# Performance work log

Hardware: AMD Instinct MI355X
Metric: run time of the kernel (lower is better)

## Reference

```python
import jax, jax.numpy as jnp
import numpy as np

D_MODEL = 1024
N_HEADS = 16
HEAD_DIM = D_MODEL // N_HEADS


def setup_inputs() -> dict:
    key = jax.random.key(0)
    ks = jax.random.split(key, 5)
    T, B = 2048, 2
    x = jax.random.normal(ks[0], (T, B, D_MODEL), dtype=jnp.float32)
    s = 1.0 / np.sqrt(D_MODEL)
    Wq = jax.random.normal(ks[1], (D_MODEL, D_MODEL), dtype=jnp.float32) * s
    Wk = jax.random.normal(ks[2], (D_MODEL, D_MODEL), dtype=jnp.float32) * s
    Wv = jax.random.normal(ks[3], (D_MODEL, D_MODEL), dtype=jnp.float32) * s
    Wo = jax.random.normal(ks[4], (D_MODEL, D_MODEL), dtype=jnp.float32) * s
    return {"x": x, "Wq": Wq, "Wk": Wk, "Wv": Wv, "Wo": Wo}


def reference(x, Wq, Wk, Wv, Wo):
    T, B, C = x.shape
    H, D = N_HEADS, HEAD_DIM

    def split_heads(t):
        # (T,B,C) -> (B,H,T,D), matching view+permute(1,2,0,3)
        return t.reshape(T, B, H, D).transpose(1, 2, 0, 3)

    q = split_heads(x @ Wq.T)
    k = split_heads(x @ Wk.T)
    v = split_heads(x @ Wv.T)

    scale = 1.0 / jnp.sqrt(jnp.asarray(D, dtype=x.dtype))
    scores = jnp.einsum('bhqd,bhkd->bhqk', q, k) * scale  # (B,H,T,T)
    causal = jnp.tril(jnp.ones((T, T), dtype=bool))
    scores = jnp.where(causal, scores, jnp.asarray(-jnp.inf, dtype=scores.dtype))
    probs = jax.nn.softmax(scores, axis=-1)
    ctx = jnp.einsum('bhqk,bhkd->bhqd', probs, v)  # (B,H,T,D)
    ctx = ctx.transpose(2, 0, 1, 3).reshape(T, B, C)
    return ctx @ Wo.T
```

## Files before the change

### kernel.cpp

```cpp
#include <hip/hip_runtime.h>
#include <hip/hip_bf16.h>

#define TT 2048
#define BB 2
#define CC 1024
#define HH 16
#define DD 64
#define MM (TT * BB)

typedef short bf16x8 __attribute__((ext_vector_type(8)));
typedef float f32x4  __attribute__((ext_vector_type(4)));

__device__ inline ushort f2b(float f) {
    union { float f; unsigned u; } v; v.f = f;
    unsigned r = v.u + 0x7FFFu + ((v.u >> 16) & 1u);
    return (ushort)(r >> 16);
}

__device__ inline unsigned pack_bf16(float a, float b) {
    __hip_bfloat162 h = __float22bfloat162_rn(make_float2(a, b));
    union { __hip_bfloat162 h; unsigned u; } c; c.h = h;
    return c.u;
}

__device__ inline void gload_lds16(const ushort* g, ushort* l) {
    __builtin_amdgcn_global_load_lds(
        (const __attribute__((address_space(1))) void*)g,
        (__attribute__((address_space(3))) void*)l, 16, 0, 0);
}

#define XQUADS (MM * CC / 4)
#define WQUADS (CC * CC / 4)
__global__ __launch_bounds__(256) void conv_all(const float* __restrict__ x,
                                                const float* __restrict__ Wq,
                                                const float* __restrict__ Wk,
                                                const float* __restrict__ Wv,
                                                const float* __restrict__ Wo,
                                                ushort* __restrict__ dst) {
    int idx = blockIdx.x * 256 + threadIdx.x;
    const float* src;
    int off;
    if (idx < XQUADS) {
        src = x; off = idx;
    } else {
        int wi = (idx - XQUADS) >> 18;
        off = (idx - XQUADS) & (WQUADS - 1);
        src = (wi == 0) ? Wq : (wi == 1) ? Wk : (wi == 2) ? Wv : Wo;
    }
    float4 v = ((const float4*)src)[off];
    ushort4 o = {f2b(v.x), f2b(v.y), f2b(v.z), f2b(v.w)};
    ((ushort4*)dst)[idx] = o;
}

__global__ __launch_bounds__(256) void gemm_qkv(const ushort* __restrict__ A,
                                                const ushort* __restrict__ B0,
                                                const ushort* __restrict__ B1,
                                                const ushort* __restrict__ B2,
                                                ushort* __restrict__ Oq,
                                                ushort* __restrict__ Ok,
                                                ushort* __restrict__ Ov) {
    __shared__ __align__(16) ushort As[128 * 32];
    __shared__ __align__(16) ushort Bs[128 * 32];

    const int tid = threadIdx.x;
    const int wave = tid >> 6, lane = tid & 63;
    const int quad = lane >> 4, l16 = lane & 15;
    const int wm = wave >> 1, wn = wave & 1;

    const int bm = blockIdx.x * 128;
    const int by = blockIdx.y;
    const int wsel = by >> 3;
    const ushort* Bp = (wsel == 0) ? B0 : (wsel == 1) ? B1 : B2;
    const int bn = (by & 7) * 128;

    const int srow = lane >> 2;
    const int scol = (lane & 3) * 8;

    f32x4 acc[4][4];
#pragma unroll
    for (int i = 0; i < 4; i++)
#pragma unroll
        for (int j = 0; j < 4; j++) acc[i][j] = (f32x4){0.f, 0.f, 0.f, 0.f};

    for (int k0 = 0; k0 < CC; k0 += 32) {
#pragma unroll
        for (int i = 0; i < 2; i++) {
            const int rbase = wave * 32 + i * 16;
            gload_lds16(A + (size_t)(bm + rbase + srow) * CC + k0 + scol,
                        As + rbase * 32);
            gload_lds16(Bp + (size_t)(bn + rbase + srow) * CC + k0 + scol,
                        Bs + rbase * 32);
        }
        __syncthreads();

        bf16x8 af[4], bf[4];
#pragma unroll
        for (int mi = 0; mi < 4; mi++)
            af[mi] = *(const bf16x8*)(As + (wm * 64 + mi * 16 + l16) * 32 + quad * 8);
#pragma unroll
        for (int ni = 0; ni < 4; ni++)
            bf[ni] = *(const bf16x8*)(Bs + (wn * 64 + ni * 16 + l16) * 32 + quad * 8);
#pragma unroll
        for (int mi = 0; mi < 4; mi++)
#pragma unroll
            for (int ni = 0; ni < 4; ni++)
                acc[mi][ni] = __builtin_amdgcn_mfma_f32_16x16x32_bf16(
                    af[mi], bf[ni], acc[mi][ni], 0, 0, 0);
        __syncthreads();
    }

#pragma unroll
    for (int mi = 0; mi < 4; mi++) {
#pragma unroll
        for (int r = 0; r < 4; r++) {
            const int m = bm + wm * 64 + mi * 16 + quad * 4 + r;
#pragma unroll
            for (int ni = 0; ni < 4; ni++) {
                const int colg = bn + wn * 64 + ni * 16 + l16;
                float v = acc[mi][ni][r];
                if (wsel == 0) v *= 0.18033688f;
                const int t = m >> 1, b = m & 1;
                const int h = colg >> 6, d = colg & 63;
                ushort* dst = (wsel == 0) ? Oq : (wsel == 1) ? Ok : Ov;
                dst[(((size_t)(b * HH + h)) * TT + t) * DD + d] = f2b(v);
            }
        }
    }
}

__global__ __launch_bounds__(256) void gemm_out(const ushort* __restrict__ A,
                                                const ushort* __restrict__ Bm,
                                                float* __restrict__ Of) {
    __shared__ __align__(16) ushort As[128 * 32];
    __shared__ __align__(16) ushort Bs[64 * 32];

    const int tid = threadIdx.x;
    const int wave = tid >> 6, lane = tid & 63;
    const int quad = lane >> 4, l16 = lane & 15;

    const int bm = blockIdx.x * 128;
    const int bn = blockIdx.y * 64;

    const int srow = lane >> 2;
    const int scol = (lane & 3) * 8;

    f32x4 acc[2][4];
#pragma unroll
    for (int i = 0; i < 2; i++)
#pragma unroll
        for (int j = 0; j < 4; j++) acc[i][j] = (f32x4){0.f, 0.f, 0.f, 0.f};

    for (int k0 = 0; k0 < CC; k0 += 32) {
#pragma unroll
        for (int i = 0; i < 2; i++) {
            const int rbase = wave * 32 + i * 16;
            gload_lds16(A + (size_t)(bm + rbase + srow) * CC + k0 + scol,
                        As + rbase * 32);
        }
        gload_lds16(Bm + (size_t)(bn + wave * 16 + srow) * CC + k0 + scol,
                    Bs + wave * 16 * 32);
        __syncthreads();

        bf16x8 af[2], bf[4];
#pragma unroll
        for (int mi = 0; mi < 2; mi++)
            af[mi] = *(const bf16x8*)(As + (wave * 32 + mi * 16 + l16) * 32 + quad * 8);
#pragma unroll
        for (int ni = 0; ni < 4; ni++)
            bf[ni] = *(const bf16x8*)(Bs + (ni * 16 + l16) * 32 + quad * 8);
#pragma unroll
        for (int mi = 0; mi < 2; mi++)
#pragma unroll
            for (int ni = 0; ni < 4; ni++)
                acc[mi][ni] = __builtin_amdgcn_mfma_f32_16x16x32_bf16(
                    af[mi], bf[ni], acc[mi][ni], 0, 0, 0);
        __syncthreads();
    }

#pragma unroll
    for (int mi = 0; mi < 2; mi++)
#pragma unroll
        for (int r = 0; r < 4; r++) {
            const int m = bm + wave * 32 + mi * 16 + quad * 4 + r;
#pragma unroll
            for (int ni = 0; ni < 4; ni++)
                Of[(size_t)m * CC + bn + ni * 16 + l16] = acc[mi][ni][r];
        }
}

__global__ __launch_bounds__(256) void prep_kv(const ushort* __restrict__ Kb,
                                               const ushort* __restrict__ Vb,
                                               ushort* __restrict__ Kf,
                                               ushort* __restrict__ Vf) {
    __shared__ __align__(16) ushort Ls[64 * 72];
    const int tile = blockIdx.x;
    const int bh   = blockIdx.y;
    const int t    = threadIdx.x;
    const size_t src = (size_t)bh * TT * DD + (size_t)tile * 64 * DD;
    const size_t dst = (size_t)bh * TT * DD + (size_t)tile * 4096;

#pragma unroll
    for (int i = 0; i < 2; i++) {
        int e = t + i * 256;
        int r = e >> 3, kc = (e & 7) * 8;
        *(uint4*)(Ls + r * 72 + kc) = *(const uint4*)(Kb + src + r * 64 + kc);
    }
    __syncthreads();
#pragma unroll
    for (int i = 0; i < 2; i++) {
        int o = t + i * 256;
        int c = o >> 8, nb = (o >> 6) & 3, lane = o & 63;
        int quad = lane >> 4, l16 = lane & 15;
        int j = nb * 16 + l16, k0 = c * 32 + quad * 8;
        *(uint4*)(Kf + dst + (size_t)o * 8) = *(const uint4*)(Ls + j * 72 + k0);
    }
    __syncthreads();

#pragma unroll
    for (int i = 0; i < 2; i++) {
        int e = t + i * 256;
        int r = e >> 3, kc = (e & 7) * 8;
        *(uint4*)(Ls + r * 72 + kc) = *(const uint4*)(Vb + src + r * 64 + kc);
    }
    __syncthreads();
#pragma unroll
    for (int i = 0; i < 2; i++) {
        int o = t + i * 256;
        int c = o >> 8, db = (o >> 6) & 3, lane = o & 63;
        int quad = lane >> 4, l16 = lane & 15;
        int d = db * 16 + l16;
        ushort tmp[8];
#pragma unroll
        for (int u = 0; u < 8; u++) {
            int jp = c * 32 + quad * 8 + u;
            int j = (jp & 3) * 16 + (jp >> 2);
            tmp[u] = Ls[j * 72 + d];
        }
        *(uint4*)(Vf + dst + (size_t)o * 8) = *(uint4*)tmp;
    }
}

template <bool DIAG>
__device__ __forceinline__ void attn_step(const bf16x8* qa, f32x4* O, float* l,
                                          const bf16x8* kf, const bf16x8* vf,
                                          ushort* P, int j0, int qbase,
                                          int quad, int l16) {
    f32x4 S[4];
#pragma unroll
    for (int nb = 0; nb < 4; nb++) S[nb] = (f32x4){0.f, 0.f, 0.f, 0.f};
#pragma unroll
    for (int c = 0; c < 2; c++)
#pragma unroll
        for (int nb = 0; nb < 4; nb++)
            S[nb] = __builtin_amdgcn_mfma_f32_16x16x32_bf16(qa[c], kf[c * 4 + nb],
                                                            S[nb], 0, 0, 0);

#pragma unroll
    for (int r = 0; r < 4; r++) {
        const int qg = qbase + quad * 4 + r;
        float p[4];
#pragma unroll
        for (int nb = 0; nb < 4; nb++) {
            float s = S[nb][r];
            if (DIAG) { if (j0 + nb * 16 + l16 > qg) s = -1e30f; }
            p[nb] = __builtin_amdgcn_exp2f(s);
        }
        l[r] += (p[0] + p[1]) + (p[2] + p[3]);
        uint2 w; w.x = pack_bf16(p[0], p[1]); w.y = pack_bf16(p[2], p[3]);
        *(uint2*)(P + (quad * 4 + r) * 72 + l16 * 4) = w;
    }

#pragma unroll
    for (int c = 0; c < 2; c++) {
        bf16x8 pa = *(const bf16x8*)(P + l16 * 72 + c * 32 + quad * 8);
#pragma unroll
        for (int db = 0; db < 4; db++)
            O[db] = __builtin_amdgcn_mfma_f32_16x16x32_bf16(pa, vf[c * 4 + db],
                                                            O[db], 0, 0, 0);
    }
}

__global__ __launch_bounds__(256, 2) void attn_mfma(const ushort* __restrict__ Qb,
                                                    const ushort* __restrict__ Kf,
                                                    const ushort* __restrict__ Vf,
                                                    ushort* __restrict__ ctx) {
    __shared__ __align__(16) ushort PsA[4 * 16 * 72];
    __shared__ __align__(16) ushort PsB[4 * 16 * 72];

    const int tid  = threadIdx.x;
    const int wave = tid >> 6;
    const int lane = tid & 63;
    const int quad = lane >> 4;
    const int l16  = lane & 15;

    const int p  = blockIdx.x;
    const int bh = blockIdx.y;
    const int qtA = p, qtB = (TT / 64 - 1) - p;
    const int q0A = qtA * 64 + wave * 16;
    const int q0B = qtB * 64 + wave * 16;

    const size_t baseQK = (size_t)bh * TT * DD;

    bf16x8 qaA[2], qaB[2];
    {
        const ushort* qp = Qb + baseQK + (size_t)(q0A + l16) * DD + quad * 8;
        qaA[0] = *(const bf16x8*)(qp);
        qaA[1] = *(const bf16x8*)(qp + 32);
        const ushort* qp2 = Qb + baseQK + (size_t)(q0B + l16) * DD + quad * 8;
        qaB[0] = *(const bf16x8*)(qp2);
        qaB[1] = *(const bf16x8*)(qp2 + 32);
    }

    f32x4 OA[4], OB[4];
#pragma unroll
    for (int i = 0; i < 4; i++) {
        OA[i] = (f32x4){0.f, 0.f, 0.f, 0.f};
        OB[i] = (f32x4){0.f, 0.f, 0.f, 0.f};
    }
    float lA[4] = {0.f, 0.f, 0.f, 0.f};
    float lB[4] = {0.f, 0.f, 0.f, 0.f};

    ushort* PA = PsA + wave * 16 * 72;
    ushort* PB = PsB + wave * 16 * 72;

    const ushort* Kfp = Kf + baseQK;
    const ushort* Vfp = Vf + baseQK;

    for (int kt = 0; kt <= qtB; kt++) {
        const int j0 = kt * 64;

        bf16x8 kf[8], vf[8];
#pragma unroll
        for (int i = 0; i < 8; i++) {
            kf[i] = *(const bf16x8*)(Kfp + (i << 9) + lane * 8);
            vf[i] = *(const bf16x8*)(Vfp + (i << 9) + lane * 8);
        }

        if (kt == qtB)
            attn_step<true >(qaB, OB, lB, kf, vf, PB, j0, q0B, quad, l16);
        else
            attn_step<false>(qaB, OB, lB, kf, vf, PB, j0, q0B, quad, l16);

        if (kt < qtA)
            attn_step<false>(qaA, OA, lA, kf, vf, PA, j0, q0A, quad, l16);
        else if (kt == qtA)
            attn_step<true >(qaA, OA, lA, kf, vf, PA, j0, q0A, quad, l16);

        Kfp += 4096;
        Vfp += 4096;
    }

    const int b = bh >> 4, h = bh & 15;
#pragma unroll
    for (int r = 0; r < 4; r++) {
        float la = lA[r], lb = lB[r];
        la += __shfl_xor(la, 1); la += __shfl_xor(la, 2);
        la += __shfl_xor(la, 4); la += __shfl_xor(la, 8);
        lb += __shfl_xor(lb, 1); lb += __shfl_xor(lb, 2);
        lb += __shfl_xor(lb, 4); lb += __shfl_xor(lb, 8);
        const float invA = 1.f / la;
        const float invB = 1.f / lb;
        const int tA = q0A + quad * 4 + r;
        const int tB = q0B + quad * 4 + r;
#pragma unroll
        for (int db = 0; db < 4; db++) {
            ctx[((size_t)tA * BB + b) * CC + h * DD + db * 16 + l16] =
                f2b(OA[db][r] * invA);
            ctx[((size_t)tB * BB + b) * CC + h * DD + db * 16 + l16] =
                f2b(OB[db][r] * invB);
        }
    }
}

extern "C" void kernel_launch(void* const* d_in, const int* in_sizes, int n_in,
                              void* d_out, int out_size, void* d_ws, size_t ws_size,
                              hipStream_t stream) {
    const float* x  = (const float*)d_in[0];
    const float* Wq = (const float*)d_in[1];
    const float* Wk = (const float*)d_in[2];
    const float* Wv = (const float*)d_in[3];
    const float* Wo = (const float*)d_in[4];
    float* out = (float*)d_out;

    ushort* xb  = (ushort*)d_ws;
    ushort* Wb  = xb + (size_t)MM * CC;
    ushort* Wqb = Wb;
    ushort* Wkb = Wb + (size_t)CC * CC;
    ushort* Wvb = Wb + 2 * (size_t)CC * CC;
    ushort* Wob = Wb + 3 * (size_t)CC * CC;
    ushort* Qb  = Wb + 4 * (size_t)CC * CC;
    ushort* Kb  = Qb + (size_t)MM * CC;
    ushort* Vb  = Kb + (size_t)MM * CC;
    ushort* Kf  = Vb + (size_t)MM * CC;
    ushort* Vf  = Kf + (size_t)MM * CC;
    ushort* Ctxb = Vf + (size_t)MM * CC;

    conv_all<<<dim3((XQUADS + 4 * WQUADS) / 256), 256, 0, stream>>>(
        x, Wq, Wk, Wv, Wo, xb);

    gemm_qkv<<<dim3(MM / 128, 24), 256, 0, stream>>>(
        xb, Wqb, Wkb, Wvb, Qb, Kb, Vb);

    prep_kv<<<dim3(TT / 64, BB * HH), 256, 0, stream>>>(Kb, Vb, Kf, Vf);

    attn_mfma<<<dim3(TT / 128, BB * HH), 256, 0, stream>>>(Qb, Kf, Vf, Ctxb);

    gemm_out<<<dim3(MM / 128, CC / 64), 256, 0, stream>>>(Ctxb, Wob, out);
}
```

Before: 176.2 us.

## Write K in fragment layout from QKV GEMM and enlarge attention query tiles

The QKV GEMM epilogue now writes K directly in the MFMA fragment layout, so prep only rearranges V and the separate K transpose pass is dropped. The attention kernel now gives each wave 32 query rows per tile (128 per block tile), which halves the grid to 8x32 blocks and doubles reuse of each loaded K/V fragment. It also prefetches the next K tile into registers while the current one is used. The cost is more register pressure (launch bounds drop to 1 block per CU), fewer blocks to spread across the GPU, and scattered K stores in the GEMM epilogue.

New measurement: 185.3 us. +5.2%, slower.

```diff
diff --git a/kernel.cpp b/kernel.cpp
--- a/kernel.cpp
+++ b/kernel.cpp
@@ -118,11 +118,21 @@
             for (int ni = 0; ni < 4; ni++) {
                 const int colg = bn + wn * 64 + ni * 16 + l16;
                 float v = acc[mi][ni][r];
-                if (wsel == 0) v *= 0.18033688f;
                 const int t = m >> 1, b = m & 1;
                 const int h = colg >> 6, d = colg & 63;
-                ushort* dst = (wsel == 0) ? Oq : (wsel == 1) ? Ok : Ov;
-                dst[(((size_t)(b * HH + h)) * TT + t) * DD + d] = f2b(v);
+                if (wsel == 0) {
+                    v *= 0.18033688f;
+                    Oq[(((size_t)(b * HH + h)) * TT + t) * DD + d] = f2b(v);
+                } else if (wsel == 1) {
+                    const int jj = t & 63;
+                    size_t idx = ((size_t)(b * HH + h) * TT) * DD
+                               + (size_t)(t >> 6) * 4096
+                               + (d >> 5) * 2048 + (jj >> 4) * 512
+                               + (((d >> 3) & 3) * 16 + (jj & 15)) * 8 + (d & 7);
+                    Ok[idx] = f2b(v);
+                } else {
+                    Ov[(((size_t)(b * HH + h)) * TT + t) * DD + d] = f2b(v);
+                }
             }
         }
     }
@@ -188,10 +198,8 @@
         }
 }
 
-__global__ __launch_bounds__(256) void prep_kv(const ushort* __restrict__ Kb,
-                                               const ushort* __restrict__ Vb,
-                                               ushort* __restrict__ Kf,
-                                               ushort* __restrict__ Vf) {
+__global__ __launch_bounds__(256) void prep_v(const ushort* __restrict__ Vb,
+                                              ushort* __restrict__ Vf) {
     __shared__ __align__(16) ushort Ls[64 * 72];
     const int tile = blockIdx.x;
     const int bh   = blockIdx.y;
@@ -203,23 +211,6 @@
     for (int i = 0; i < 2; i++) {
         int e = t + i * 256;
         int r = e >> 3, kc = (e & 7) * 8;
-        *(uint4*)(Ls + r * 72 + kc) = *(const uint4*)(Kb + src + r * 64 + kc);
-    }
-    __syncthreads();
-#pragma unroll
-    for (int i = 0; i < 2; i++) {
-        int o = t + i * 256;
-        int c = o >> 8, nb = (o >> 6) & 3, lane = o & 63;
-        int quad = lane >> 4, l16 = lane & 15;
-        int j = nb * 16 + l16, k0 = c * 32 + quad * 8;
-        *(uint4*)(Kf + dst + (size_t)o * 8) = *(const uint4*)(Ls + j * 72 + k0);
-    }
-    __syncthreads();
-
-#pragma unroll
-    for (int i = 0; i < 2; i++) {
-        int e = t + i * 256;
-        int r = e >> 3, kc = (e & 7) * 8;
         *(uint4*)(Ls + r * 72 + kc) = *(const uint4*)(Vb + src + r * 64 + kc);
     }
     __syncthreads();
@@ -240,136 +231,186 @@
     }
 }
 
-template <bool DIAG>
-__device__ __forceinline__ void attn_step(const bf16x8* qa, f32x4* O, float* l,
-                                          const bf16x8* kf, const bf16x8* vf,
-                                          ushort* P, int j0, int qbase,
-                                          int quad, int l16) {
-    f32x4 S[4];
-#pragma unroll
-    for (int nb = 0; nb < 4; nb++) S[nb] = (f32x4){0.f, 0.f, 0.f, 0.f};
-#pragma unroll
-    for (int c = 0; c < 2; c++)
-#pragma unroll
-        for (int nb = 0; nb < 4; nb++)
-            S[nb] = __builtin_amdgcn_mfma_f32_16x16x32_bf16(qa[c], kf[c * 4 + nb],
-                                                            S[nb], 0, 0, 0);
-
-#pragma unroll
-    for (int r = 0; r < 4; r++) {
-        const int qg = qbase + quad * 4 + r;
-        float p[4];
-#pragma unroll
-        for (int nb = 0; nb < 4; nb++) {
-            float s = S[nb][r];
-            if (DIAG) { if (j0 + nb * 16 + l16 > qg) s = -1e30f; }
-            p[nb] = __builtin_amdgcn_exp2f(s);
-        }
-        l[r] += (p[0] + p[1]) + (p[2] + p[3]);
-        uint2 w; w.x = pack_bf16(p[0], p[1]); w.y = pack_bf16(p[2], p[3]);
-        *(uint2*)(P + (quad * 4 + r) * 72 + l16 * 4) = w;
-    }
-
-#pragma unroll
-    for (int c = 0; c < 2; c++) {
-        bf16x8 pa = *(const bf16x8*)(P + l16 * 72 + c * 32 + quad * 8);
-#pragma unroll
-        for (int db = 0; db < 4; db++)
-            O[db] = __builtin_amdgcn_mfma_f32_16x16x32_bf16(pa, vf[c * 4 + db],
-                                                            O[db], 0, 0, 0);
-    }
-}
-
-__global__ __launch_bounds__(256, 2) void attn_mfma(const ushort* __restrict__ Qb,
+__global__ __launch_bounds__(256, 1) void attn_mfma(const ushort* __restrict__ Qb,
                                                     const ushort* __restrict__ Kf,
                                                     const ushort* __restrict__ Vf,
                                                     ushort* __restrict__ ctx) {
-    __shared__ __align__(16) ushort PsA[4 * 16 * 72];
-    __shared__ __align__(16) ushort PsB[4 * 16 * 72];
+    __shared__ __align__(16) ushort PsA[4 * 32 * 72];
+    __shared__ __align__(16) ushort PsB[4 * 32 * 72];
 
     const int tid  = threadIdx.x;
-    const int wave = tid >> 6;
+    const int wave = __builtin_amdgcn_readfirstlane(tid >> 6);
     const int lane = tid & 63;
     const int quad = lane >> 4;
     const int l16  = lane & 15;
 
     const int p  = blockIdx.x;
     const int bh = blockIdx.y;
-    const int qtA = p, qtB = (TT / 64 - 1) - p;
-    const int q0A = qtA * 64 + wave * 16;
-    const int q0B = qtB * 64 + wave * 16;
+    const int qtA = p, qtB = 15 - p;
+    const int q0A = qtA * 128 + wave * 32;
+    const int q0B = qtB * 128 + wave * 32;
+    const int kdA = q0A >> 6;
+    const int kdB = q0B >> 6;
 
     const size_t baseQK = (size_t)bh * TT * DD;
 
-    bf16x8 qaA[2], qaB[2];
-    {
-        const ushort* qp = Qb + baseQK + (size_t)(q0A + l16) * DD + quad * 8;
-        qaA[0] = *(const bf16x8*)(qp);
-        qaA[1] = *(const bf16x8*)(qp + 32);
-        const ushort* qp2 = Qb + baseQK + (size_t)(q0B + l16) * DD + quad * 8;
-        qaB[0] = *(const bf16x8*)(qp2);
-        qaB[1] = *(const bf16x8*)(qp2 + 32);
-    }
-
-    f32x4 OA[4], OB[4];
-#pragma unroll
-    for (int i = 0; i < 4; i++) {
-        OA[i] = (f32x4){0.f, 0.f, 0.f, 0.f};
-        OB[i] = (f32x4){0.f, 0.f, 0.f, 0.f};
-    }
-    float lA[4] = {0.f, 0.f, 0.f, 0.f};
-    float lB[4] = {0.f, 0.f, 0.f, 0.f};
-
-    ushort* PA = PsA + wave * 16 * 72;
-    ushort* PB = PsB + wave * 16 * 72;
+    bf16x8 qaA[2][2], qaB[2][2];
+#pragma unroll
+    for (int ms = 0; ms < 2; ms++) {
+        const ushort* qp = Qb + baseQK + (size_t)(q0A + ms * 16 + l16) * DD + quad * 8;
+        qaA[ms][0] = *(const bf16x8*)(qp);
+        qaA[ms][1] = *(const bf16x8*)(qp + 32);
+        const ushort* qp2 = Qb + baseQK + (size_t)(q0B + ms * 16 + l16) * DD + quad * 8;
+        qaB[ms][0] = *(const bf16x8*)(qp2);
+        qaB[ms][1] = *(const bf16x8*)(qp2 + 32);
+    }
+
+    f32x4 OA[2][4], OB[2][4];
+#pragma unroll
+    for (int ms = 0; ms < 2; ms++)
+#pragma unroll
+        for (int db = 0; db < 4; db++) {
+            OA[ms][db] = (f32x4){0.f, 0.f, 0.f, 0.f};
+            OB[ms][db] = (f32x4){0.f, 0.f, 0.f, 0.f};
+        }
+    float lA[2][4] = {{0.f}}, lB[2][4] = {{0.f}};
+
+    ushort* PA = PsA + wave * 32 * 72;
+    ushort* PB = PsB + wave * 32 * 72;
 
     const ushort* Kfp = Kf + baseQK;
     const ushort* Vfp = Vf + baseQK;
 
-    for (int kt = 0; kt <= qtB; kt++) {
+    bf16x8 kfc[8], kfn[8], vf[8];
+#pragma unroll
+    for (int i = 0; i < 8; i++) kfc[i] = *(const bf16x8*)(Kfp + (i << 9) + lane * 8);
+
+    for (int kt = 0; kt <= kdB; kt++) {
         const int j0 = kt * 64;
-
-        bf16x8 kf[8], vf[8];
-#pragma unroll
-        for (int i = 0; i < 8; i++) {
-            kf[i] = *(const bf16x8*)(Kfp + (i << 9) + lane * 8);
-            vf[i] = *(const bf16x8*)(Vfp + (i << 9) + lane * 8);
-        }
-
-        if (kt == qtB)
-            attn_step<true >(qaB, OB, lB, kf, vf, PB, j0, q0B, quad, l16);
-        else
-            attn_step<false>(qaB, OB, lB, kf, vf, PB, j0, q0B, quad, l16);
-
-        if (kt < qtA)
-            attn_step<false>(qaA, OA, lA, kf, vf, PA, j0, q0A, quad, l16);
-        else if (kt == qtA)
-            attn_step<true >(qaA, OA, lA, kf, vf, PA, j0, q0A, quad, l16);
-
-        Kfp += 4096;
-        Vfp += 4096;
+        const bool doA = (kt <= kdA);
+        const bool dgA = (kt == kdA);
+        const bool dgB = (kt == kdB);
+
+#pragma unroll
+        for (int i = 0; i < 8; i++)
+            vf[i] = *(const bf16x8*)(Vfp + ((size_t)kt << 12) + (i << 9) + lane * 8);
+        if (kt < kdB) {
+#pragma unroll
+            for (int i = 0; i < 8; i++)
+                kfn[i] = *(const bf16x8*)(Kfp + (((size_t)kt + 1) << 12) + (i << 9) + lane * 8);
+        }
+
+        f32x4 S[2][4];
+#pragma unroll
+        for (int ms = 0; ms < 2; ms++)
+#pragma unroll
+            for (int nb = 0; nb < 4; nb++) S[ms][nb] = (f32x4){0.f, 0.f, 0.f, 0.f};
+#pragma unroll
+        for (int c = 0; c < 2; c++)
+#pragma unroll
+            for (int ms = 0; ms < 2; ms++)
+#pragma unroll
+                for (int nb = 0; nb < 4; nb++)
+                    S[ms][nb] = __builtin_amdgcn_mfma_f32_16x16x32_bf16(
+                        qaB[ms][c], kfc[c * 4 + nb], S[ms][nb], 0, 0, 0);
+
+#pragma unroll
+        for (int ms = 0; ms < 2; ms++)
+#pragma unroll
+            for (int r = 0; r < 4; r++) {
+                const int qg = q0B + ms * 16 + quad * 4 + r;
+                float pv[4];
+#pragma unroll
+                for (int nb = 0; nb < 4; nb++) {
+                    float s = S[ms][nb][r];
+                    if (dgB) { if (j0 + nb * 16 + l16 > qg) s = -1e30f; }
+                    pv[nb] = __builtin_amdgcn_exp2f(s);
+                }
+                lB[ms][r] += (pv[0] + pv[1]) + (pv[2] + pv[3]);
+                uint2 w; w.x = pack_bf16(pv[0], pv[1]); w.y = pack_bf16(pv[2], pv[3]);
+                *(uint2*)(PB + (ms * 16 + quad * 4 + r) * 72 + l16 * 4) = w;
+            }
+
+        if (doA) {
+#pragma unroll
+            for (int ms = 0; ms < 2; ms++)
+#pragma unroll
+                for (int nb = 0; nb < 4; nb++) S[ms][nb] = (f32x4){0.f, 0.f, 0.f, 0.f};
+#pragma unroll
+            for (int c = 0; c < 2; c++)
+#pragma unroll
+                for (int ms = 0; ms < 2; ms++)
+#pragma unroll
+                    for (int nb = 0; nb < 4; nb++)
+                        S[ms][nb] = __builtin_amdgcn_mfma_f32_16x16x32_bf16(
+                            qaA[ms][c], kfc[c * 4 + nb], S[ms][nb], 0, 0, 0);
+#pragma unroll
+            for (int ms = 0; ms < 2; ms++)
+#pragma unroll
+                for (int r = 0; r < 4; r++) {
+                    const int qg = q0A + ms * 16 + quad * 4 + r;
+                    float pv[4];
+#pragma unroll
+                    for (int nb = 0; nb < 4; nb++) {
+                        float s = S[ms][nb][r];
+                        if (dgA) { if (j0 + nb * 16 + l16 > qg) s = -1e30f; }
+                        pv[nb] = __builtin_amdgcn_exp2f(s);
+                    }
+                    lA[ms][r] += (pv[0] + pv[1]) + (pv[2] + pv[3]);
+                    uint2 w; w.x = pack_bf16(pv[0], pv[1]); w.y = pack_bf16(pv[2], pv[3]);
+                    *(uint2*)(PA + (ms * 16 + quad * 4 + r) * 72 + l16 * 4) = w;
+                }
+        }
+
+#pragma unroll
+        for (int c = 0; c < 2; c++) {
+            bf16x8 pa0 = *(const bf16x8*)(PB + (l16) * 72 + c * 32 + quad * 8);
+            bf16x8 pa1 = *(const bf16x8*)(PB + (16 + l16) * 72 + c * 32 + quad * 8);
+#pragma unroll
+            for (int db = 0; db < 4; db++) {
+                OB[0][db] = __builtin_amdgcn_mfma_f32_16x16x32_bf16(pa0, vf[c * 4 + db], OB[0][db], 0, 0, 0);
+                OB[1][db] = __builtin_amdgcn_mfma_f32_16x16x32_bf16(pa1, vf[c * 4 + db], OB[1][db], 0, 0, 0);
+            }
+        }
+        if (doA) {
+#pragma unroll
+            for (int c = 0; c < 2; c++) {
+                bf16x8 pa0 = *(const bf16x8*)(PA + (l16) * 72 + c * 32 + quad * 8);
+                bf16x8 pa1 = *(const bf16x8*)(PA + (16 + l16) * 72 + c * 32 + quad * 8);
+#pragma unroll
+                for (int db = 0; db < 4; db++) {
+                    OA[0][db] = __builtin_amdgcn_mfma_f32_16x16x32_bf16(pa0, vf[c * 4 + db], OA[0][db], 0, 0, 0);
+                    OA[1][db] = __builtin_amdgcn_mfma_f32_16x16x32_bf16(pa1, vf[c * 4 + db], OA[1][db], 0, 0, 0);
+                }
+            }
+        }
+
+#pragma unroll
+        for (int i = 0; i < 8; i++) kfc[i] = kfn[i];
     }
 
     const int b = bh >> 4, h = bh & 15;
 #pragma unroll
-    for (int r = 0; r < 4; r++) {
-        float la = lA[r], lb = lB[r];
-        la += __shfl_xor(la, 1); la += __shfl_xor(la, 2);
-        la += __shfl_xor(la, 4); la += __shfl_xor(la, 8);
-        lb += __shfl_xor(lb, 1); lb += __shfl_xor(lb, 2);
-        lb += __shfl_xor(lb, 4); lb += __shfl_xor(lb, 8);
-        const float invA = 1.f / la;
-        const float invB = 1.f / lb;
-        const int tA = q0A + quad * 4 + r;
-        const int tB = q0B + quad * 4 + r;
-#pragma unroll
-        for (int db = 0; db < 4; db++) {
-            ctx[((size_t)tA * BB + b) * CC + h * DD + db * 16 + l16] =
-                f2b(OA[db][r] * invA);
-            ctx[((size_t)tB * BB + b) * CC + h * DD + db * 16 + l16] =
-                f2b(OB[db][r] * invB);
-        }
-    }
+    for (int ms = 0; ms < 2; ms++)
+#pragma unroll
+        for (int r = 0; r < 4; r++) {
+            float la = lA[ms][r], lb = lB[ms][r];
+            la += __shfl_xor(la, 1); la += __shfl_xor(la, 2);
+            la += __shfl_xor(la, 4); la += __shfl_xor(la, 8);
+            lb += __shfl_xor(lb, 1); lb += __shfl_xor(lb, 2);
+            lb += __shfl_xor(lb, 4); lb += __shfl_xor(lb, 8);
+            const float invA = 1.f / la;
+            const float invB = 1.f / lb;
+            const int tA = q0A + ms * 16 + quad * 4 + r;
+            const int tB = q0B + ms * 16 + quad * 4 + r;
+#pragma unroll
+            for (int db = 0; db < 4; db++) {
+                ctx[((size_t)tA * BB + b) * CC + h * DD + db * 16 + l16] =
+                    f2b(OA[ms][db][r] * invA);
+                ctx[((size_t)tB * BB + b) * CC + h * DD + db * 16 + l16] =
+                    f2b(OB[ms][db][r] * invB);
+            }
+        }
 }
 
 extern "C" void kernel_launch(void* const* d_in, const int* in_sizes, int n_in,
@@ -389,21 +430,20 @@
     ushort* Wvb = Wb + 2 * (size_t)CC * CC;
     ushort* Wob = Wb + 3 * (size_t)CC * CC;
     ushort* Qb  = Wb + 4 * (size_t)CC * CC;
-    ushort* Kb  = Qb + (size_t)MM * CC;
-    ushort* Vb  = Kb + (size_t)MM * CC;
-    ushort* Kf  = Vb + (size_t)MM * CC;
-    ushort* Vf  = Kf + (size_t)MM * CC;
+    ushort* Kf  = Qb + (size_t)MM * CC;
+    ushort* Vb  = Kf + (size_t)MM * CC;
+    ushort* Vf  = Vb + (size_t)MM * CC;
     ushort* Ctxb = Vf + (size_t)MM * CC;
 
     conv_all<<<dim3((XQUADS + 4 * WQUADS) / 256), 256, 0, stream>>>(
         x, Wq, Wk, Wv, Wo, xb);
 
     gemm_qkv<<<dim3(MM / 128, 24), 256, 0, stream>>>(
-        xb, Wqb, Wkb, Wvb, Qb, Kb, Vb);
-
-    prep_kv<<<dim3(TT / 64, BB * HH), 256, 0, stream>>>(Kb, Vb, Kf, Vf);
-
-    attn_mfma<<<dim3(TT / 128, BB * HH), 256, 0, stream>>>(Qb, Kf, Vf, Ctxb);
+        xb, Wqb, Wkb, Wvb, Qb, Kf, Vb);
+
+    prep_v<<<dim3(TT / 64, BB * HH), 256, 0, stream>>>(Vb, Vf);
+
+    attn_mfma<<<dim3(8, BB * HH), 256, 0, stream>>>(Qb, Kf, Vf, Ctxb);
 
     gemm_out<<<dim3(MM / 128, CC / 64), 256, 0, stream>>>(Ctxb, Wob, out);
 }
```

## Fuse K/V fragment relayout into QKV GEMM epilogue, drop prep_kv kernel

Applied to the files above, without the earlier changes.

The QKV GEMM epilogue now writes K directly in the MFMA fragment layout the attention kernel expects, and stages V tiles through shared memory to write them in the permuted fragment layout. This removes the separate prep_kv kernel launch along with its extra read and write of K and V through global memory. In exchange, the epilogue gains extra LDS traffic and syncs for V blocks, and K stores become scattered 2-byte writes, which may hurt coalescing.

Result: slower. 183.9 us (+4.4%).

```diff
diff --git a/kernel.cpp b/kernel.cpp
--- a/kernel.cpp
+++ b/kernel.cpp
@@ -59,8 +59,9 @@
                                                 ushort* __restrict__ Oq,
                                                 ushort* __restrict__ Ok,
                                                 ushort* __restrict__ Ov) {
-    __shared__ __align__(16) ushort As[128 * 32];
-    __shared__ __align__(16) ushort Bs[128 * 32];
+    __shared__ __align__(16) ushort smem[8704];
+    ushort* As = smem;
+    ushort* Bs = smem + 4096;
 
     const int tid = threadIdx.x;
     const int wave = tid >> 6, lane = tid & 63;
@@ -109,20 +110,70 @@
         __syncthreads();
     }
 
-#pragma unroll
-    for (int mi = 0; mi < 4; mi++) {
-#pragma unroll
-        for (int r = 0; r < 4; r++) {
-            const int m = bm + wm * 64 + mi * 16 + quad * 4 + r;
-#pragma unroll
-            for (int ni = 0; ni < 4; ni++) {
-                const int colg = bn + wn * 64 + ni * 16 + l16;
-                float v = acc[mi][ni][r];
-                if (wsel == 0) v *= 0.18033688f;
-                const int t = m >> 1, b = m & 1;
-                const int h = colg >> 6, d = colg & 63;
-                ushort* dst = (wsel == 0) ? Oq : (wsel == 1) ? Ok : Ov;
-                dst[(((size_t)(b * HH + h)) * TT + t) * DD + d] = f2b(v);
+    if (wsel < 2) {
+#pragma unroll
+        for (int mi = 0; mi < 4; mi++) {
+#pragma unroll
+            for (int r = 0; r < 4; r++) {
+                const int m = bm + wm * 64 + mi * 16 + quad * 4 + r;
+#pragma unroll
+                for (int ni = 0; ni < 4; ni++) {
+                    const int colg = bn + wn * 64 + ni * 16 + l16;
+                    float v = acc[mi][ni][r];
+                    const int t = m >> 1, b = m & 1;
+                    const int h = colg >> 6, d = colg & 63;
+                    if (wsel == 0) {
+                        v *= 0.18033688f;
+                        Oq[(((size_t)(b * HH + h)) * TT + t) * DD + d] = f2b(v);
+                    } else {
+                        const int jj = t & 63;
+                        size_t idx = ((size_t)(b * HH + h) * TT) * DD
+                                   + (size_t)(t >> 6) * 4096
+                                   + (d >> 5) * 2048 + (jj >> 4) * 512
+                                   + (((d >> 3) & 3) * 16 + (jj & 15)) * 8 + (d & 7);
+                        Ok[idx] = f2b(v);
+                    }
+                }
+            }
+        }
+    } else {
+        const int tile = blockIdx.x;
+#pragma unroll
+        for (int bpass = 0; bpass < 2; bpass++) {
+            __syncthreads();
+#pragma unroll
+            for (int mi = 0; mi < 4; mi++)
+#pragma unroll
+                for (int r = 0; r < 4; r++) {
+                    if ((r & 1) != bpass) continue;
+                    const int mrel = wm * 64 + mi * 16 + quad * 4 + r;
+                    const int t_loc = mrel >> 1;
+#pragma unroll
+                    for (int ni = 0; ni < 4; ni++) {
+                        const int n_local = wn * 64 + ni * 16 + l16;
+                        smem[t_loc * 136 + n_local] = f2b(acc[mi][ni][r]);
+                    }
+                }
+            __syncthreads();
+#pragma unroll
+            for (int i = 0; i < 4; i++) {
+                const int og = tid + i * 256;
+                const int hl = og >> 9;
+                const int o  = og & 511;
+                const int c  = o >> 8, db = (o >> 6) & 3, lo = o & 63;
+                const int qo = lo >> 4, l16o = lo & 15;
+                const int d  = db * 16 + l16o;
+                ushort tmp[8];
+#pragma unroll
+                for (int u = 0; u < 8; u++) {
+                    const int jp = c * 32 + qo * 8 + u;
+                    const int j  = (jp & 3) * 16 + (jp >> 2);
+                    tmp[u] = smem[j * 136 + hl * 64 + d];
+                }
+                const int h = (bn >> 6) + hl;
+                const size_t dstb = ((size_t)(bpass * HH + h) * TT) * DD
+                                  + (size_t)tile * 4096;
+                *(uint4*)(Ov + dstb + (size_t)o * 8) = *(uint4*)tmp;
             }
         }
     }
@@ -186,58 +237,6 @@
             for (int ni = 0; ni < 4; ni++)
                 Of[(size_t)m * CC + bn + ni * 16 + l16] = acc[mi][ni][r];
         }
-}
-
-__global__ __launch_bounds__(256) void prep_kv(const ushort* __restrict__ Kb,
-                                               const ushort* __restrict__ Vb,
-                                               ushort* __restrict__ Kf,
-                                               ushort* __restrict__ Vf) {
-    __shared__ __align__(16) ushort Ls[64 * 72];
-    const int tile = blockIdx.x;
-    const int bh   = blockIdx.y;
-    const int t    = threadIdx.x;
-    const size_t src = (size_t)bh * TT * DD + (size_t)tile * 64 * DD;
-    const size_t dst = (size_t)bh * TT * DD + (size_t)tile * 4096;
-
-#pragma unroll
-    for (int i = 0; i < 2; i++) {
-        int e = t + i * 256;
-        int r = e >> 3, kc = (e & 7) * 8;
-        *(uint4*)(Ls + r * 72 + kc) = *(const uint4*)(Kb + src + r * 64 + kc);
-    }
-    __syncthreads();
-#pragma unroll
-    for (int i = 0; i < 2; i++) {
-        int o = t + i * 256;
-        int c = o >> 8, nb = (o >> 6) & 3, lane = o & 63;
-        int quad = lane >> 4, l16 = lane & 15;
-        int j = nb * 16 + l16, k0 = c * 32 + quad * 8;
-        *(uint4*)(Kf + dst + (size_t)o * 8) = *(const uint4*)(Ls + j * 72 + k0);
-    }
-    __syncthreads();
-
-#pragma unroll
-    for (int i = 0; i < 2; i++) {
-        int e = t + i * 256;
-        int r = e >> 3, kc = (e & 7) * 8;
-        *(uint4*)(Ls + r * 72 + kc) = *(const uint4*)(Vb + src + r * 64 + kc);
-    }
-    __syncthreads();
-#pragma unroll
-    for (int i = 0; i < 2; i++) {
-        int o = t + i * 256;
-        int c = o >> 8, db = (o >> 6) & 3, lane = o & 63;
-        int quad = lane >> 4, l16 = lane & 15;
-        int d = db * 16 + l16;
-        ushort tmp[8];
-#pragma unroll
-        for (int u = 0; u < 8; u++) {
-            int jp = c * 32 + quad * 8 + u;
-            int j = (jp & 3) * 16 + (jp >> 2);
-            tmp[u] = Ls[j * 72 + d];
-        }
-        *(uint4*)(Vf + dst + (size_t)o * 8) = *(uint4*)tmp;
-    }
 }
 
 template <bool DIAG>
@@ -389,9 +388,7 @@
     ushort* Wvb = Wb + 2 * (size_t)CC * CC;
     ushort* Wob = Wb + 3 * (size_t)CC * CC;
     ushort* Qb  = Wb + 4 * (size_t)CC * CC;
-    ushort* Kb  = Qb + (size_t)MM * CC;
-    ushort* Vb  = Kb + (size_t)MM * CC;
-    ushort* Kf  = Vb + (size_t)MM * CC;
+    ushort* Kf  = Qb + (size_t)MM * CC;
     ushort* Vf  = Kf + (size_t)MM * CC;
     ushort* Ctxb = Vf + (size_t)MM * CC;
 
@@ -399,11 +396,9 @@
         x, Wq, Wk, Wv, Wo, xb);
 
     gemm_qkv<<<dim3(MM / 128, 24), 256, 0, stream>>>(
-        xb, Wqb, Wkb, Wvb, Qb, Kb, Vb);
-
-    prep_kv<<<dim3(TT / 64, BB * HH), 256, 0, stream>>>(Kb, Vb, Kf, Vf);
-
-    attn_mfma<<<dim3(TT / 128, BB * HH), 256, 0, stream>>>(Qb, Kf, Vf, Ctxb);
+        xb, Wqb, Wkb, Wvb, Qb, Kf, Vf);
+
+    attn_mfma<<<dim3(16, BB * HH), 256, 0, stream>>>(Qb, Kf, Vf, Ctxb);
 
     gemm_out<<<dim3(MM / 128, CC / 64), 256, 0, stream>>>(Ctxb, Wob, out);
 }
```

## Split attention KV loop across two blocks and fuse K relayout into QKV GEMM

Applied to the files above, without the earlier changes.

The GEMM epilogue for K now writes directly into the MFMA-fragment layout, so prep_kv only has to rearrange V. The attention grid doubles: each block handles even or odd key tiles, writes unnormalized partial outputs and row sums in fp32, and a new combine kernel sums the two halves and normalizes into the bf16 context. Launch bounds are raised to allow more waves per SIMD. The goal is better CU occupancy and less relayout traffic, at the cost of an extra launch and fp32 partial-result traffic. With no running max, the softmax reduction stays a plain sum, so the two halves can be added directly.

Result: slower. 267.4 us (+51.8%).

```diff
diff --git a/kernel.cpp b/kernel.cpp
--- a/kernel.cpp
+++ b/kernel.cpp
@@ -118,11 +118,21 @@
             for (int ni = 0; ni < 4; ni++) {
                 const int colg = bn + wn * 64 + ni * 16 + l16;
                 float v = acc[mi][ni][r];
-                if (wsel == 0) v *= 0.18033688f;
                 const int t = m >> 1, b = m & 1;
                 const int h = colg >> 6, d = colg & 63;
-                ushort* dst = (wsel == 0) ? Oq : (wsel == 1) ? Ok : Ov;
-                dst[(((size_t)(b * HH + h)) * TT + t) * DD + d] = f2b(v);
+                if (wsel == 0) {
+                    v *= 0.18033688f;
+                    Oq[(((size_t)(b * HH + h)) * TT + t) * DD + d] = f2b(v);
+                } else if (wsel == 1) {
+                    const int jj = t & 63;
+                    size_t idx = ((size_t)(b * HH + h) * TT) * DD
+                               + (size_t)(t >> 6) * 4096
+                               + (d >> 5) * 2048 + (jj >> 4) * 512
+                               + (((d >> 3) & 3) * 16 + (jj & 15)) * 8 + (d & 7);
+                    Ok[idx] = f2b(v);
+                } else {
+                    Ov[(((size_t)(b * HH + h)) * TT + t) * DD + d] = f2b(v);
+                }
             }
         }
     }
@@ -188,10 +198,8 @@
         }
 }
 
-__global__ __launch_bounds__(256) void prep_kv(const ushort* __restrict__ Kb,
-                                               const ushort* __restrict__ Vb,
-                                               ushort* __restrict__ Kf,
-                                               ushort* __restrict__ Vf) {
+__global__ __launch_bounds__(256) void prep_v(const ushort* __restrict__ Vb,
+                                              ushort* __restrict__ Vf) {
     __shared__ __align__(16) ushort Ls[64 * 72];
     const int tile = blockIdx.x;
     const int bh   = blockIdx.y;
@@ -203,23 +211,6 @@
     for (int i = 0; i < 2; i++) {
         int e = t + i * 256;
         int r = e >> 3, kc = (e & 7) * 8;
-        *(uint4*)(Ls + r * 72 + kc) = *(const uint4*)(Kb + src + r * 64 + kc);
-    }
-    __syncthreads();
-#pragma unroll
-    for (int i = 0; i < 2; i++) {
-        int o = t + i * 256;
-        int c = o >> 8, nb = (o >> 6) & 3, lane = o & 63;
-        int quad = lane >> 4, l16 = lane & 15;
-        int j = nb * 16 + l16, k0 = c * 32 + quad * 8;
-        *(uint4*)(Kf + dst + (size_t)o * 8) = *(const uint4*)(Ls + j * 72 + k0);
-    }
-    __syncthreads();
-
-#pragma unroll
-    for (int i = 0; i < 2; i++) {
-        int e = t + i * 256;
-        int r = e >> 3, kc = (e & 7) * 8;
         *(uint4*)(Ls + r * 72 + kc) = *(const uint4*)(Vb + src + r * 64 + kc);
     }
     __syncthreads();
@@ -280,10 +271,11 @@
     }
 }
 
-__global__ __launch_bounds__(256, 2) void attn_mfma(const ushort* __restrict__ Qb,
+__global__ __launch_bounds__(256, 4) void attn_mfma(const ushort* __restrict__ Qb,
                                                     const ushort* __restrict__ Kf,
                                                     const ushort* __restrict__ Vf,
-                                                    ushort* __restrict__ ctx) {
+                                                    float* __restrict__ Opart,
+                                                    float* __restrict__ Lpart) {
     __shared__ __align__(16) ushort PsA[4 * 16 * 72];
     __shared__ __align__(16) ushort PsB[4 * 16 * 72];
 
@@ -293,9 +285,11 @@
     const int quad = lane >> 4;
     const int l16  = lane & 15;
 
-    const int p  = blockIdx.x;
+    const int bx = blockIdx.x;
+    const int p  = bx >> 1;
+    const int kp = bx & 1;
     const int bh = blockIdx.y;
-    const int qtA = p, qtB = (TT / 64 - 1) - p;
+    const int qtA = p, qtB = 31 - p;
     const int q0A = qtA * 64 + wave * 16;
     const int q0B = qtB * 64 + wave * 16;
 
@@ -323,11 +317,13 @@
     ushort* PA = PsA + wave * 16 * 72;
     ushort* PB = PsB + wave * 16 * 72;
 
-    const ushort* Kfp = Kf + baseQK;
-    const ushort* Vfp = Vf + baseQK;
-
-    for (int kt = 0; kt <= qtB; kt++) {
+    const ushort* Kfb = Kf + baseQK;
+    const ushort* Vfb = Vf + baseQK;
+
+    for (int kt = kp; kt <= qtB; kt += 2) {
         const int j0 = kt * 64;
+        const ushort* Kfp = Kfb + ((size_t)kt << 12);
+        const ushort* Vfp = Vfb + ((size_t)kt << 12);
 
         bf16x8 kf[8], vf[8];
 #pragma unroll
@@ -345,31 +341,69 @@
             attn_step<false>(qaA, OA, lA, kf, vf, PA, j0, q0A, quad, l16);
         else if (kt == qtA)
             attn_step<true >(qaA, OA, lA, kf, vf, PA, j0, q0A, quad, l16);
-
-        Kfp += 4096;
-        Vfp += 4096;
-    }
-
-    const int b = bh >> 4, h = bh & 15;
+    }
+
+    const size_t obA = (((size_t)bh * 32 + qtA) * 2 + kp) * 4096;
+    const size_t obB = (((size_t)bh * 32 + qtB) * 2 + kp) * 4096;
+    const size_t lbA = (((size_t)bh * 32 + qtA) * 2 + kp) * 64;
+    const size_t lbB = (((size_t)bh * 32 + qtB) * 2 + kp) * 64;
 #pragma unroll
     for (int r = 0; r < 4; r++) {
+        const int row = wave * 16 + quad * 4 + r;
         float la = lA[r], lb = lB[r];
         la += __shfl_xor(la, 1); la += __shfl_xor(la, 2);
         la += __shfl_xor(la, 4); la += __shfl_xor(la, 8);
         lb += __shfl_xor(lb, 1); lb += __shfl_xor(lb, 2);
         lb += __shfl_xor(lb, 4); lb += __shfl_xor(lb, 8);
-        const float invA = 1.f / la;
-        const float invB = 1.f / lb;
-        const int tA = q0A + quad * 4 + r;
-        const int tB = q0B + quad * 4 + r;
+        if (l16 == 0) {
+            Lpart[lbA + row] = la;
+            Lpart[lbB + row] = lb;
+        }
 #pragma unroll
         for (int db = 0; db < 4; db++) {
-            ctx[((size_t)tA * BB + b) * CC + h * DD + db * 16 + l16] =
-                f2b(OA[db][r] * invA);
-            ctx[((size_t)tB * BB + b) * CC + h * DD + db * 16 + l16] =
-                f2b(OB[db][r] * invB);
-        }
-    }
+            Opart[obA + (size_t)row * 64 + db * 16 + l16] = OA[db][r];
+            Opart[obB + (size_t)row * 64 + db * 16 + l16] = OB[db][r];
+        }
+    }
+}
+
+__global__ __launch_bounds__(256) void attn_combine(const float* __restrict__ Opart,
+                                                    const float* __restrict__ Lpart,
+                                                    ushort* __restrict__ ctx) {
+    const int qt = blockIdx.x;
+    const int bh = blockIdx.y;
+    const int tid = threadIdx.x;
+    const int row = tid >> 2;
+    const int cg  = (tid & 3) * 16;
+
+    const size_t b0 = (((size_t)bh * 32 + qt) * 2 + 0) * 4096;
+    const size_t b1 = b0 + 4096;
+    const size_t l0 = (((size_t)bh * 32 + qt) * 2 + 0) * 64;
+
+    const float l = Lpart[l0 + row] + Lpart[l0 + 64 + row];
+    const float inv = 1.f / l;
+
+    float4 o0[4], o1[4];
+#pragma unroll
+    for (int i = 0; i < 4; i++) {
+        o0[i] = *(const float4*)(Opart + b0 + (size_t)row * 64 + cg + i * 4);
+        o1[i] = *(const float4*)(Opart + b1 + (size_t)row * 64 + cg + i * 4);
+    }
+
+    ushort tmp[16];
+#pragma unroll
+    for (int i = 0; i < 4; i++) {
+        tmp[i * 4 + 0] = f2b((o0[i].x + o1[i].x) * inv);
+        tmp[i * 4 + 1] = f2b((o0[i].y + o1[i].y) * inv);
+        tmp[i * 4 + 2] = f2b((o0[i].z + o1[i].z) * inv);
+        tmp[i * 4 + 3] = f2b((o0[i].w + o1[i].w) * inv);
+    }
+
+    const int t = qt * 64 + row;
+    const int b = bh >> 4, h = bh & 15;
+    ushort* dst = ctx + ((size_t)t * BB + b) * CC + h * DD + cg;
+    *(uint4*)(dst)     = *(uint4*)(tmp);
+    *(uint4*)(dst + 8) = *(uint4*)(tmp + 8);
 }
 
 extern "C" void kernel_launch(void* const* d_in, const int* in_sizes, int n_in,
@@ -389,21 +423,24 @@
     ushort* Wvb = Wb + 2 * (size_t)CC * CC;
     ushort* Wob = Wb + 3 * (size_t)CC * CC;
     ushort* Qb  = Wb + 4 * (size_t)CC * CC;
-    ushort* Kb  = Qb + (size_t)MM * CC;
-    ushort* Vb  = Kb + (size_t)MM * CC;
-    ushort* Kf  = Vb + (size_t)MM * CC;
-    ushort* Vf  = Kf + (size_t)MM * CC;
+    ushort* Kf  = Qb + (size_t)MM * CC;
+    ushort* Vb  = Kf + (size_t)MM * CC;
+    ushort* Vf  = Vb + (size_t)MM * CC;
     ushort* Ctxb = Vf + (size_t)MM * CC;
+    float*  Opart = (float*)(Ctxb + (size_t)MM * CC);
+    float*  Lpart = Opart + (size_t)32 * 32 * 2 * 4096;
 
     conv_all<<<dim3((XQUADS + 4 * WQUADS) / 256), 256, 0, stream>>>(
         x, Wq, Wk, Wv, Wo, xb);
 
     gemm_qkv<<<dim3(MM / 128, 24), 256, 0, stream>>>(
-        xb, Wqb, Wkb, Wvb, Qb, Kb, Vb);
-
-    prep_kv<<<dim3(TT / 64, BB * HH), 256, 0, stream>>>(Kb, Vb, Kf, Vf);
-
-    attn_mfma<<<dim3(TT / 128, BB * HH), 256, 0, stream>>>(Qb, Kf, Vf, Ctxb);
+        xb, Wqb, Wkb, Wvb, Qb, Kf, Vb);
+
+    prep_v<<<dim3(TT / 64, BB * HH), 256, 0, stream>>>(Vb, Vf);
+
+    attn_mfma<<<dim3(32, BB * HH), 256, 0, stream>>>(Qb, Kf, Vf, Opart, Lpart);
+
+    attn_combine<<<dim3(TT / 64, BB * HH), 256, 0, stream>>>(Opart, Lpart, Ctxb);
 
     gemm_out<<<dim3(MM / 128, CC / 64), 256, 0, stream>>>(Ctxb, Wob, out);
 }
```
